# Kernel tuning notes

Hardware: AMD Instinct MI355X
Metric: run time of the kernel (lower is better)

The kernel has to match this reference:

```python
import jax, jax.numpy as jnp
import numpy as np

B, N, K = 16, 1024, 20
EPS = 1e-5

def _lin_init(key, fan_in, fan_out):
    k1, k2 = jax.random.split(key)
    s = 1.0 / np.sqrt(fan_in)
    W = jax.random.uniform(k1, (fan_in, fan_out), minval=-s, maxval=s, dtype=jnp.float32)
    b = jax.random.uniform(k2, (fan_out,), minval=-s, maxval=s, dtype=jnp.float32)
    return W, b

def setup_inputs() -> dict:
    key = jax.random.key(0)
    ks = jax.random.split(key, 12)
    pos = jax.random.normal(ks[0], (B * N, 3), dtype=jnp.float32)
    batch = jnp.repeat(jnp.arange(B, dtype=jnp.int64), N)
    W1a, b1a = _lin_init(ks[1], 6, 64);    W1b, b1b = _lin_init(ks[2], 64, 64)
    W2a, b2a = _lin_init(ks[3], 128, 64);  W2b, b2b = _lin_init(ks[4], 64, 64)
    W3a, b3a = _lin_init(ks[5], 128, 128); W3b, b3b = _lin_init(ks[6], 128, 128)
    W4a, b4a = _lin_init(ks[7], 256, 256); W4b, b4b = _lin_init(ks[8], 256, 256)
    lin1_w, lin1_b = _lin_init(ks[9], 512, 1024)
    gamma = jnp.ones((1024,), jnp.float32); beta = jnp.zeros((1024,), jnp.float32)
    lin2_w, lin2_b = _lin_init(ks[10], 1024, 40)
    return dict(pos=pos, batch=batch,
                W1a=W1a, b1a=b1a, W1b=W1b, b1b=b1b,
                W2a=W2a, b2a=b2a, W2b=W2b, b2b=b2b,
                W3a=W3a, b3a=b3a, W3b=W3b, b3b=b3b,
                W4a=W4a, b4a=b4a, W4b=W4b, b4b=b4b,
                lin1_w=lin1_w, lin1_b=lin1_b, gamma=gamma, beta=beta,
                lin2_w=lin2_w, lin2_b=lin2_b)

def _edge_conv(x, Wa, ba, Wb, bb):
    # x: [B, N, C]. Dynamic kNN in feature space (per cloud, self included,
    # matching PyG knn), edge feature [x_i, x_j - x_i], MLP, max-aggregate.
    sq = jnp.sum(x * x, axis=-1)                                   # [B,N]
    d = sq[:, :, None] - 2.0 * jnp.einsum('bnc,bmc->bnm', x, x) + sq[:, None, :]
    _, idx = jax.lax.top_k(-d, K)                                  # [B,N,K]
    xj = jax.vmap(lambda xb, ib: xb[ib])(x, idx)                   # [B,N,K,C]
    xi = jnp.broadcast_to(x[:, :, None, :], xj.shape)
    e = jnp.concatenate([xi, xj - xi], axis=-1)                    # [B,N,K,2C]
    h = jax.nn.relu(e @ Wa + ba) @ Wb + bb                         # [B,N,K,Co]
    return jnp.max(h, axis=2)                                      # [B,N,Co]

def reference(pos, batch, W1a, b1a, W1b, b1b, W2a, b2a, W2b, b2b,
              W3a, b3a, W3b, b3b, W4a, b4a, W4b, b4b,
              lin1_w, lin1_b, gamma, beta, lin2_w, lin2_b):
    del batch  # clouds are equal-sized: batch == repeat(arange(B), N)
    x = pos.reshape(B, N, 3)
    x1 = _edge_conv(x,  W1a, b1a, W1b, b1b)   # [B,N,64]
    x2 = _edge_conv(x1, W2a, b2a, W2b, b2b)   # [B,N,64]
    x3 = _edge_conv(x2, W3a, b3a, W3b, b3b)   # [B,N,128]
    x4 = _edge_conv(x3, W4a, b4a, W4b, b4b)   # [B,N,256]
    x_cat = jnp.concatenate([x1, x2, x3, x4], axis=-1)  # [B,N,512]
    pooled = jnp.max(x_cat, axis=1)                      # global_max_pool -> [B,512]
    h = pooled @ lin1_w + lin1_b                         # [B,1024]
    mu = jnp.mean(h, axis=0)
    var = jnp.mean((h - mu) ** 2, axis=0)                # biased, as PyTorch BN
    h = (h - mu) * jax.lax.rsqrt(var + EPS) * gamma + beta
    h = jax.nn.relu(h)                                   # dropout is identity in eval
    logits = h @ lin2_w + lin2_b                         # [B,40]
    return jax.nn.log_softmax(logits, axis=1)
```

## Files before the change

kernel.cpp:

```cpp
#include <hip/hip_runtime.h>
#include <hip/hip_bf16.h>
#include <hip/hip_fp16.h>

#define B_   16
#define N_   1024
#define KNN  20
#define NP   (B_ * N_)

typedef short bf16x8 __attribute__((ext_vector_type(8)));
typedef _Float16 half8 __attribute__((ext_vector_type(8)));
typedef float f32x4  __attribute__((ext_vector_type(4)));
typedef float f32x16 __attribute__((ext_vector_type(16)));

__device__ __forceinline__ unsigned short f2bf(float f) {
  unsigned u = __float_as_uint(f);
  u += 0x7fffu + ((u >> 16) & 1u);
  return (unsigned short)(u >> 16);
}

__global__ __launch_bounds__(256) void pairdist_kernel(
    const float* __restrict__ X, int LD, int coff, int C,
    unsigned* __restrict__ Dk) {
  __shared__ __align__(16) char pd_smem[64 * 68 * 4];
  __shared__ float sqi_s[64], sqj_s[64];
  float (*Xi)[68] = (float(*)[68])pd_smem;
  float (*Xj)[68] = (float(*)[68])(pd_smem + 32 * 68 * 4);
  unsigned (*Tt)[68] = (unsigned(*)[68])pd_smem;
  int lin = blockIdx.x, by = 0;
  while (lin >= 16 - by) { lin -= 16 - by; ++by; }
  int bx = by + lin;
  int b  = blockIdx.z;
  int i0 = by * 64, j0 = bx * 64;
  int t  = threadIdx.x;
  int tx = t & 15, ty = t >> 4;
  int cx = t & 31, ry = t >> 5;
  float acc[4][4] = {};
  float sqacc = 0.f;
  for (int c0 = 0; c0 < C; c0 += 32) {
    int cc = min(32, C - c0);
    if (cx < cc) {
      for (int r = ry; r < 64; r += 8) {
        Xi[cx][r] = X[(size_t)(b * N_ + i0 + r) * LD + coff + c0 + cx];
        Xj[cx][r] = X[(size_t)(b * N_ + j0 + r) * LD + coff + c0 + cx];
      }
    }
    __syncthreads();
    if (t < 64) {
      for (int c = 0; c < cc; ++c) sqacc = fmaf(Xi[c][t], Xi[c][t], sqacc);
    } else if (t < 128) {
      int r = t - 64;
      for (int c = 0; c < cc; ++c) sqacc = fmaf(Xj[c][r], Xj[c][r], sqacc);
    }
    for (int c = 0; c < cc; ++c) {
      float4 a4 = *(const float4*)&Xi[c][ty * 4];
      float4 b4 = *(const float4*)&Xj[c][tx * 4];
      float a[4] = {a4.x, a4.y, a4.z, a4.w};
      float bb[4] = {b4.x, b4.y, b4.z, b4.w};
#pragma unroll
      for (int p = 0; p < 4; ++p)
#pragma unroll
        for (int q = 0; q < 4; ++q)
          acc[p][q] = fmaf(a[p], bb[q], acc[p][q]);
    }
    __syncthreads();
  }
  if (t < 64) sqi_s[t] = sqacc;
  else if (t < 128) sqj_s[t - 64] = sqacc;
  __syncthreads();
  float sqi[4], sqj[4];
#pragma unroll
  for (int p = 0; p < 4; ++p) sqi[p] = sqi_s[ty * 4 + p];
#pragma unroll
  for (int q = 0; q < 4; ++q) sqj[q] = sqj_s[tx * 4 + q];
  bool offdiag = (bx > by);
#pragma unroll
  for (int p = 0; p < 4; ++p) {
    uint4 st;
    unsigned* kk = (unsigned*)&st;
#pragma unroll
    for (int q = 0; q < 4; ++q) {
      float d = fmaxf((sqi[p] - 2.f * acc[p][q]) + sqj[q], 0.f);
      unsigned db = __float_as_uint(d) & 0xFFFFFC00u;
      kk[q] = db | (unsigned)(j0 + tx * 4 + q);
      if (offdiag)
        Tt[tx * 4 + q][ty * 4 + p] = db | (unsigned)(i0 + ty * 4 + p);
    }
    *(uint4*)&Dk[(size_t)(b * N_ + i0 + ty * 4 + p) * N_ + j0 + tx * 4] = st;
  }
  if (offdiag) {
    __syncthreads();
#pragma unroll
    for (int p = 0; p < 4; ++p) {
      *(uint4*)&Dk[(size_t)(b * N_ + j0 + ty * 4 + p) * N_ + i0 + tx * 4] =
          *(uint4*)&Tt[ty * 4 + p][tx * 4];
    }
  }
}

template<int C>
__global__ __launch_bounds__(256) void sqc_kernel(
    const float* __restrict__ X, int coff, float* __restrict__ sq) {
  int w = threadIdx.x >> 6, lane = threadIdx.x & 63;
  int pt = blockIdx.x * 4 + w;
  const float* xr = X + (size_t)pt * 512 + coff;
  float s = 0.f;
  for (int c = lane; c < C; c += 64) s = fmaf(xr[c], xr[c], s);
#pragma unroll
  for (int off = 32; off >= 1; off >>= 1) s += __shfl_xor(s, off);
  if (lane == 0) sq[pt] = s;
}

template<int C>
__global__ __launch_bounds__(256) void gramt_kernel(
    const float* __restrict__ X, int coff, const float* __restrict__ sqv,
    unsigned* __restrict__ Dk) {
  constexpr int KP = C / 64;
  __shared__ __align__(16) unsigned short Phi[64 * 64], Plo[64 * 64];
  __shared__ __align__(16) unsigned short Qhi[64 * 64], Qlo[64 * 64];
  int tid = threadIdx.x, wv = tid >> 6, lane = tid & 63;
  int rc = lane & 31, half = lane >> 5;
  int ti = blockIdx.x & 15, tj = blockIdx.x >> 4;
  int b  = blockIdx.z;
  int qi = wv >> 1, qj = wv & 1;
  f32x16 acc = {};
#pragma unroll
  for (int kp = 0; kp < KP; ++kp) {
    if (kp) __syncthreads();
#pragma unroll
    for (int it = 0; it < 4; ++it) {
      int u = tid + it * 256;
      int side = u >> 9;
      int row  = (u >> 3) & 63;
      int slot = u & 7;
      int grow = b * N_ + (side ? tj : ti) * 64 + row;
      const float* xr = X + (size_t)grow * 512 + coff + kp * 64 + slot * 8;
      float4 x0 = *(const float4*)xr;
      float4 x1 = *(const float4*)(xr + 4);
      float xs[8] = {x0.x, x0.y, x0.z, x0.w, x1.x, x1.y, x1.z, x1.w};
      union { half8 v; _Float16 h[8]; } H, L;
#pragma unroll
      for (int q = 0; q < 8; ++q) {
        _Float16 hv = (_Float16)xs[q];
        H.h[q] = hv;
        L.h[q] = (_Float16)(xs[q] - (float)hv);
      }
      int off = row * 64 + (slot ^ (row & 7)) * 8;
      if (side) { *(half8*)&Qhi[off] = H.v; *(half8*)&Qlo[off] = L.v; }
      else      { *(half8*)&Phi[off] = H.v; *(half8*)&Plo[off] = L.v; }
    }
    __syncthreads();
#pragma unroll
    for (int ch = 0; ch < 4; ++ch) {
      int s = ch * 2 + half;
      int arow = qi * 32 + rc, brow = qj * 32 + rc;
      int aoff = arow * 64 + (s ^ (arow & 7)) * 8;
      int boff = brow * 64 + (s ^ (brow & 7)) * 8;
      half8 Ah = *(const half8*)&Phi[aoff];
      half8 Al = *(const half8*)&Plo[aoff];
      half8 Bh = *(const half8*)&Qhi[boff];
      half8 Bl = *(const half8*)&Qlo[boff];
      acc = __builtin_amdgcn_mfma_f32_32x32x16_f16(Ah, Bh, acc, 0, 0, 0);
      acc = __builtin_amdgcn_mfma_f32_32x32x16_f16(Al, Bh, acc, 0, 0, 0);
      acc = __builtin_amdgcn_mfma_f32_32x32x16_f16(Ah, Bl, acc, 0, 0, 0);
    }
  }
  int gj = tj * 64 + qj * 32 + rc;
  float sqj = sqv[b * N_ + gj];
#pragma unroll
  for (int e = 0; e < 16; ++e) {
    int gi = ti * 64 + qi * 32 + (e & 3) + 8 * (e >> 2) + 4 * half;
    float sqi = sqv[b * N_ + gi];
    float d = fmaxf(sqi - 2.f * acc[e] + sqj, 0.f);
    if (gi == gj) d = 0.f;
    Dk[(size_t)(b * N_ + gi) * N_ + gj] =
        (__float_as_uint(d) & 0xFFFFFC00u) | (unsigned)gj;
  }
}

__device__ __forceinline__ unsigned wave_min_bcast(unsigned x) {
  unsigned t;
  t = (unsigned)__builtin_amdgcn_update_dpp(-1, (int)x, 0x111, 0xF, 0xF, false);
  x = min(x, t);
  t = (unsigned)__builtin_amdgcn_update_dpp(-1, (int)x, 0x112, 0xF, 0xF, false);
  x = min(x, t);
  t = (unsigned)__builtin_amdgcn_update_dpp(-1, (int)x, 0x114, 0xF, 0xF, false);
  x = min(x, t);
  t = (unsigned)__builtin_amdgcn_update_dpp(-1, (int)x, 0x118, 0xF, 0xF, false);
  x = min(x, t);
  t = (unsigned)__builtin_amdgcn_update_dpp(-1, (int)x, 0x142, 0xF, 0xF, false);
  x = min(x, t);
  t = (unsigned)__builtin_amdgcn_update_dpp(-1, (int)x, 0x143, 0xF, 0xF, false);
  x = min(x, t);
  return (unsigned)__builtin_amdgcn_readlane((int)x, 63);
}

__global__ __launch_bounds__(256) void topk_kernel(
    const unsigned* __restrict__ Dk, int* __restrict__ idx) {
  int w = threadIdx.x >> 6, lane = threadIdx.x & 63;
  int p = blockIdx.x * 4 + w;
  const unsigned* row = Dk + (size_t)p * N_;
  unsigned key[16];
#pragma unroll
  for (int s = 0; s < 16; ++s) key[s] = row[lane + 64 * s];
  int base = p & ~(N_ - 1);
  for (int k = 0; k < KNN; ++k) {
    unsigned m = key[0];
#pragma unroll
    for (int s = 1; s < 16; ++s) m = min(m, key[s]);
    unsigned gm = wave_min_bcast(m);
    int j = (int)(gm & 1023u);
    if (lane == 0) idx[p * KNN + k] = base + j;
    if ((j & 63) == lane) key[j >> 6] = 0xFFFFFFFFu;
  }
}

__global__ __launch_bounds__(256) void transform_kernel(
    const float* __restrict__ X, int LD, int coff, int Cin, int Cmid,
    const float* __restrict__ Wa, const float* __restrict__ ba,
    unsigned short* __restrict__ u, unsigned short* __restrict__ v) {
  __shared__ float xs[16 * 128];
  int w = threadIdx.x >> 6, lane = threadIdx.x & 63;
  int m  = blockIdx.y * 64 + lane;
  int p0 = blockIdx.x * 16;
  for (int i = threadIdx.x; i < 16 * Cin; i += 256) {
    int pt = i / Cin, c = i - pt * Cin;
    xs[pt * Cin + c] = X[(size_t)(p0 + pt) * LD + coff + c];
  }
  __syncthreads();
  const float* xw = xs + (w * 4) * Cin;
  float ua[4] = {0.f, 0.f, 0.f, 0.f}, va[4] = {0.f, 0.f, 0.f, 0.f};
  for (int c = 0; c < Cin; ++c) {
    float wt = Wa[(size_t)c * Cmid + m];
    float wb = Wa[(size_t)(Cin + c) * Cmid + m];
    float wd = wt - wb;
#pragma unroll
    for (int i = 0; i < 4; ++i) {
      float xv = xw[i * Cin + c];
      ua[i] = fmaf(xv, wd, ua[i]);
      va[i] = fmaf(xv, wb, va[i]);
    }
  }
  float bias = ba[m];
#pragma unroll
  for (int i = 0; i < 4; ++i) {
    u[(size_t)(p0 + w * 4 + i) * Cmid + m] = f2bf(ua[i] + bias);
    v[(size_t)(p0 + w * 4 + i) * Cmid + m] = f2bf(va[i]);
  }
}

__global__ __launch_bounds__(256) void cvtwa_swz_kernel(
    const float* __restrict__ A2, const float* __restrict__ A3,
    const float* __restrict__ A4,
    unsigned short* __restrict__ d2, unsigned short* __restrict__ b2,
    unsigned short* __restrict__ d3, unsigned short* __restrict__ b3,
    unsigned short* __restrict__ d4, unsigned short* __restrict__ b4) {
  int z = blockIdx.z;
  const float* Wa; unsigned short *wd, *wb; int Cin, Cmid;
  if (z == 0)      { Wa = A2; wd = d2; wb = b2; Cin = 64;  Cmid = 64;  }
  else if (z == 1) { Wa = A3; wd = d3; wb = b3; Cin = 64;  Cmid = 128; }
  else             { Wa = A4; wd = d4; wb = b4; Cin = 128; Cmid = 256; }
  int KC = Cin / 16;
  int NC = (Cmid / 32) * KC * 64;
  int ci = blockIdx.x * 256 + threadIdx.x;
  if (ci >= NC) return;
  int ntc = ci >> 6, lane = ci & 63;
  int nt = ntc / KC, c = ntc - nt * KC;
  int n  = nt * 32 + (lane & 31);
  int kb = c * 16 + (lane >> 5) * 8;
#pragma unroll
  for (int j = 0; j < 8; ++j) {
    float top = Wa[(size_t)(kb + j) * Cmid + n];
    float bot = Wa[(size_t)(Cin + kb + j) * Cmid + n];
    wd[(size_t)ci * 8 + j] = f2bf(top - bot);
    wb[(size_t)ci * 8 + j] = f2bf(bot);
  }
}

template<int Cin, int Cmid>
__global__ __launch_bounds__(256) void transform_mfma_kernel(
    const float* __restrict__ X, int LD, int coff,
    const unsigned short* __restrict__ wdf, const unsigned short* __restrict__ wbf,
    const float* __restrict__ ba,
    unsigned short* __restrict__ u, unsigned short* __restrict__ v) {
  constexpr int KC = Cin / 16;
  int wv = threadIdx.x >> 6, lane = threadIdx.x & 63;
  int row = lane & 31, half = lane >> 5;
  int p0 = blockIdx.x * 128 + wv * 32;
  int nt = blockIdx.y;

  bf16x8 afr[KC];
  const float* xr = X + (size_t)(p0 + row) * LD + coff + half * 8;
#pragma unroll
  for (int c = 0; c < KC; ++c) {
    float4 x0 = *(const float4*)(xr + c * 16);
    float4 x1 = *(const float4*)(xr + c * 16 + 4);
    union { bf16x8 vec; __hip_bfloat162 h[4]; } pk;
    pk.h[0] = __float22bfloat162_rn({x0.x, x0.y});
    pk.h[1] = __float22bfloat162_rn({x0.z, x0.w});
    pk.h[2] = __float22bfloat162_rn({x1.x, x1.y});
    pk.h[3] = __float22bfloat162_rn({x1.z, x1.w});
    afr[c] = pk.vec;
  }

  const unsigned short* wdl = wdf + ((size_t)nt * KC * 64 + lane) * 8;
  const unsigned short* wbl = wbf + ((size_t)nt * KC * 64 + lane) * 8;
  f32x16 au = {}, av = {};
#pragma unroll
  for (int c = 0; c < KC; ++c) {
    bf16x8 bd = *(const bf16x8*)(wdl + (size_t)c * 512);
    au = __builtin_amdgcn_mfma_f32_32x32x16_bf16(afr[c], bd, au, 0, 0, 0);
  }
#pragma unroll
  for (int c = 0; c < KC; ++c) {
    bf16x8 bv = *(const bf16x8*)(wbl + (size_t)c * 512);
    av = __builtin_amdgcn_mfma_f32_32x32x16_bf16(afr[c], bv, av, 0, 0, 0);
  }

  int m = nt * 32 + row;
  float bias = ba[m];
#pragma unroll
  for (int e = 0; e < 16; ++e) {
    int orow = (e & 3) + 8 * (e >> 2) + 4 * half;
    u[(size_t)(p0 + orow) * Cmid + m] = f2bf(au[e] + bias);
    v[(size_t)(p0 + orow) * Cmid + m] = f2bf(av[e]);
  }
}

__global__ __launch_bounds__(256) void cvtw4_kernel(
    const float* __restrict__ W0, const float* __restrict__ W1,
    const float* __restrict__ W2, const float* __restrict__ W3,
    unsigned short* __restrict__ o0, unsigned short* __restrict__ o1,
    unsigned short* __restrict__ o2, unsigned short* __restrict__ o3) {
  __shared__ unsigned short tile[32][33];
  int z = blockIdx.z;
  const float* W; unsigned short* out; int Cmid, Cout;
  if (z == 0)      { W = W0; out = o0; Cmid = 64;  Cout = 64;  }
  else if (z == 1) { W = W1; out = o1; Cmid = 64;  Cout = 64;  }
  else if (z == 2) { W = W2; out = o2; Cmid = 128; Cout = 128; }
  else             { W = W3; out = o3; Cmid = 256; Cout = 256; }
  int c0 = blockIdx.x * 32, co0 = blockIdx.y * 32;
  if (c0 >= Cmid || co0 >= Cout) return;
  int tx = threadIdx.x & 31, ty = threadIdx.x >> 5;
  for (int r = ty; r < 32; r += 8)
    tile[r][tx] = f2bf(W[(size_t)(c0 + r) * Cout + co0 + tx]);
  __syncthreads();
  for (int r = ty; r < 32; r += 8)
    out[(size_t)(co0 + r) * Cmid + c0 + tx] = tile[tx][r];
}

template<int Cmid, int Cout, int CG>
__global__ __launch_bounds__(960, 3) void edge_mlp_kernel(
    const unsigned short* __restrict__ u, const unsigned short* __restrict__ v,
    const int* __restrict__ idx,
    const unsigned short* __restrict__ wbt, const float* __restrict__ bb,
    float* __restrict__ xcat, int coff) {
  constexpr int AP = Cmid + 8;
  constexpr int T  = CG / 32;
  constexpr int KC = Cmid / 16;
  constexpr int G  = Cout / CG;
  __shared__ __align__(16) unsigned short W_lds[CG * AP];
  __shared__ float qmax[120 * CG];
  int tid = threadIdx.x, w = tid >> 6, lane = tid & 63;
  int col = lane & 31, half = lane >> 5;

  int rg = blockIdx.x * 480 + w * 32 + col;
  int rgc = min(rg, NP * KNN - 1);
  int p  = rgc / 20;
  int j  = idx[rgc];
  const unsigned short* up = u + (size_t)p * Cmid + half * 8;
  const unsigned short* vp = v + (size_t)j * Cmid + half * 8;

  bf16x8 afr[KC];
#pragma unroll
  for (int c = 0; c < KC; ++c) {
    union { int4 i; __hip_bfloat162 h[4]; bf16x8 vec; } U, V, R;
    U.i = *(const int4*)(up + c * 16);
    V.i = *(const int4*)(vp + c * 16);
#pragma unroll
    for (int q = 0; q < 4; ++q) {
      float2 a = __bfloat1622float2(U.h[q]);
      float2 b = __bfloat1622float2(V.h[q]);
      R.h[q] = __float22bfloat162_rn({fmaxf(a.x + b.x, 0.f), fmaxf(a.y + b.y, 0.f)});
    }
    afr[c] = R.vec;
  }

  int brow = col * AP + half * 8;

  for (int g = 0; g < G; ++g) {
    __syncthreads();
    for (int i = tid; i < CG * (Cmid / 8); i += 960) {
      int rr = i / (Cmid / 8), q = i - rr * (Cmid / 8);
      *(int4*)&W_lds[rr * AP + q * 8] =
          *(const int4*)&wbt[(size_t)(g * CG + rr) * Cmid + q * 8];
    }
    __syncthreads();
    f32x16 acc[T] = {};
#pragma unroll
    for (int c = 0; c < KC; ++c) {
#pragma unroll
      for (int t = 0; t < T; ++t) {
        bf16x8 bf = *(const bf16x8*)&W_lds[brow + t * 32 * AP + c * 16];
        acc[t] = __builtin_amdgcn_mfma_f32_32x32x16_bf16(afr[c], bf, acc[t], 0, 0, 0);
      }
    }
#pragma unroll
    for (int t = 0; t < T; ++t) {
#pragma unroll
      for (int Q = 0; Q < 4; ++Q) {
        float m0 = fmaxf(fmaxf(acc[t][4 * Q], acc[t][4 * Q + 1]),
                         fmaxf(acc[t][4 * Q + 2], acc[t][4 * Q + 3]));
        qmax[(w * 8 + 2 * Q + half) * CG + t * 32 + col] = m0;
      }
    }
    __syncthreads();
    for (int i = tid; i < 24 * CG; i += 960) {
      int pl = i / CG, c2 = i - pl * CG;
      int pg = blockIdx.x * 24 + pl;
      if (pg < NP) {
        float mm = qmax[(pl * 5 + 0) * CG + c2];
#pragma unroll
        for (int qq = 1; qq < 5; ++qq) mm = fmaxf(mm, qmax[(pl * 5 + qq) * CG + c2]);
        xcat[(size_t)pg * 512 + coff + g * CG + c2] = mm + bb[g * CG + c2];
      }
    }
  }
}

__global__ __launch_bounds__(256) void pool1_kernel(const float* __restrict__ xcat,
                                                    float* __restrict__ part) {
  int b = blockIdx.x, g = blockIdx.y, t = threadIdx.x;
  const float* base = xcat + ((size_t)b * N_ + g * 128) * 512 + t * 2;
  float mx = -__builtin_inff(), my = -__builtin_inff();
#pragma unroll 4
  for (int r = 0; r < 128; ++r) {
    float2 vv = *(const float2*)(base + (size_t)r * 512);
    mx = fmaxf(mx, vv.x);
    my = fmaxf(my, vv.y);
  }
  *(float2*)&part[((size_t)b * 8 + g) * 512 + t * 2] = make_float2(mx, my);
}

__global__ __launch_bounds__(256) void pool2_kernel(const float* __restrict__ part,
                                                    float* __restrict__ pooled) {
  int b = blockIdx.x, t = threadIdx.x;
  float2 m = *(const float2*)&part[(size_t)b * 8 * 512 + t * 2];
#pragma unroll
  for (int g = 1; g < 8; ++g) {
    float2 vv = *(const float2*)&part[((size_t)b * 8 + g) * 512 + t * 2];
    m.x = fmaxf(m.x, vv.x);
    m.y = fmaxf(m.y, vv.y);
  }
  *(float2*)&pooled[b * 512 + t * 2] = m;
}

__global__ __launch_bounds__(256) void lin1_kernel(const float* __restrict__ pooled,
                                                   const float* __restrict__ W,
                                                   const float* __restrict__ bias,
                                                   float* __restrict__ h) {
  int flat = blockIdx.x * 256 + threadIdx.x;
  int b = flat >> 10, m = flat & 1023;
  float s = 0.f;
  for (int c = 0; c < 512; ++c) s = fmaf(pooled[b * 512 + c], W[(size_t)c * 1024 + m], s);
  h[flat] = s + bias[m];
}

__global__ __launch_bounds__(256) void bn_kernel(const float* __restrict__ h,
                                                 const float* __restrict__ gamma,
                                                 const float* __restrict__ beta,
                                                 float* __restrict__ h2) {
  int m = blockIdx.x * 256 + threadIdx.x;
  float s = 0.f;
  for (int b = 0; b < 16; ++b) s += h[b * 1024 + m];
  float mu = s * (1.f / 16.f);
  float vv = 0.f;
  for (int b = 0; b < 16; ++b) { float d = h[b * 1024 + m] - mu; vv = fmaf(d, d, vv); }
  vv *= (1.f / 16.f);
  float rstd = rsqrtf(vv + 1e-5f);
  float g = gamma[m] * rstd, be = beta[m];
  for (int b = 0; b < 16; ++b) {
    float val = (h[b * 1024 + m] - mu) * g + be;
    h2[b * 1024 + m] = fmaxf(val, 0.f);
  }
}

__global__ __launch_bounds__(64) void lin2_kernel(const float* __restrict__ h2,
                                                  const float* __restrict__ W,
                                                  const float* __restrict__ bias,
                                                  float* __restrict__ out) {
  int b = blockIdx.x, lane = threadIdx.x;
  float logit = 0.f;
  if (lane < 40) {
    logit = bias[lane];
    for (int c = 0; c < 1024; ++c)
      logit = fmaf(h2[b * 1024 + c], W[(size_t)c * 40 + lane], logit);
  }
  float mv = (lane < 40) ? logit : -__builtin_inff();
#pragma unroll
  for (int off = 32; off >= 1; off >>= 1) mv = fmaxf(mv, __shfl_xor(mv, off));
  float e = (lane < 40) ? expf(logit - mv) : 0.f;
#pragma unroll
  for (int off = 32; off >= 1; off >>= 1) e += __shfl_xor(e, off);
  float lse = mv + logf(e);
  if (lane < 40) out[b * 40 + lane] = logit - lse;
}

extern "C" void kernel_launch(void* const* d_in, const int* in_sizes, int n_in,
                              void* d_out, int out_size, void* d_ws, size_t ws_size,
                              hipStream_t stream) {
  const float* pos    = (const float*)d_in[0];
  const float* W1a = (const float*)d_in[2];  const float* b1a = (const float*)d_in[3];
  const float* W1b = (const float*)d_in[4];  const float* b1b = (const float*)d_in[5];
  const float* W2a = (const float*)d_in[6];  const float* b2a = (const float*)d_in[7];
  const float* W2b = (const float*)d_in[8];  const float* b2b = (const float*)d_in[9];
  const float* W3a = (const float*)d_in[10]; const float* b3a = (const float*)d_in[11];
  const float* W3b = (const float*)d_in[12]; const float* b3b = (const float*)d_in[13];
  const float* W4a = (const float*)d_in[14]; const float* b4a = (const float*)d_in[15];
  const float* W4b = (const float*)d_in[16]; const float* b4b = (const float*)d_in[17];
  const float* lin1_w = (const float*)d_in[18]; const float* lin1_b = (const float*)d_in[19];
  const float* gamma  = (const float*)d_in[20]; const float* beta   = (const float*)d_in[21];
  const float* lin2_w = (const float*)d_in[22]; const float* lin2_b = (const float*)d_in[23];
  float* out = (float*)d_out;

  char* ws = (char*)d_ws;
  size_t off = 0;
  auto alloc = [&](size_t bytes) {
    void* p = ws + off; off += (bytes + 255) & ~(size_t)255; return p;
  };
  float*    xcat = (float*)alloc((size_t)NP * 512 * 4);
  unsigned* Dk   = (unsigned*)alloc((size_t)NP * N_ * 4);
  int*      idx  = (int*)alloc((size_t)NP * KNN * 4);
  unsigned short* wbt1 = (unsigned short*)alloc(64 * 64 * 2);
  unsigned short* wbt2 = (unsigned short*)alloc(64 * 64 * 2);
  unsigned short* wbt3 = (unsigned short*)alloc(128 * 128 * 2);
  unsigned short* wbt4 = (unsigned short*)alloc(256 * 256 * 2);
  unsigned short* wd2 = (unsigned short*)alloc(64 * 64 * 2);
  unsigned short* wb2 = (unsigned short*)alloc(64 * 64 * 2);
  unsigned short* wd3 = (unsigned short*)alloc(64 * 128 * 2);
  unsigned short* wb3 = (unsigned short*)alloc(64 * 128 * 2);
  unsigned short* wd4 = (unsigned short*)alloc(128 * 256 * 2);
  unsigned short* wb4 = (unsigned short*)alloc(128 * 256 * 2);
  float* h      = (float*)alloc(16 * 1024 * 4);
  float* h2     = (float*)alloc(16 * 1024 * 4);
  float* pooled = (float*)alloc(16 * 512 * 4);
  float* part   = (float*)alloc(16 * 8 * 512 * 4);
  float* sqv    = (float*)alloc((size_t)NP * 4);
  unsigned short* u = (unsigned short*)Dk;
  unsigned short* v = (unsigned short*)Dk + (size_t)NP * 256;

  cvtw4_kernel<<<dim3(8, 8, 4), 256, 0, stream>>>(W1b, W2b, W3b, W4b,
                                                  wbt1, wbt2, wbt3, wbt4);
  cvtwa_swz_kernel<<<dim3(16, 1, 3), 256, 0, stream>>>(W2a, W3a, W4a,
                                                       wd2, wb2, wd3, wb3, wd4, wb4);

  dim3 pd_grid(136, 1, 16);
  dim3 gr_grid(256, 1, 16);
  const int EB = (NP * KNN + 479) / 480;
  pairdist_kernel<<<pd_grid, 256, 0, stream>>>(pos, 3, 0, 3, Dk);
  topk_kernel<<<NP / 4, 256, 0, stream>>>(Dk, idx);
  transform_kernel<<<dim3(NP / 16, 1), 256, 0, stream>>>(pos, 3, 0, 3, 64, W1a, b1a, u, v);
  edge_mlp_kernel<64, 64, 64><<<EB, 960, 0, stream>>>(u, v, idx, wbt1, b1b, xcat, 0);
  sqc_kernel<64><<<NP / 4, 256, 0, stream>>>(xcat, 0, sqv);
  gramt_kernel<64><<<gr_grid, 256, 0, stream>>>(xcat, 0, sqv, Dk);
  topk_kernel<<<NP / 4, 256, 0, stream>>>(Dk, idx);
  transform_mfma_kernel<64, 64><<<dim3(NP / 128, 2), 256, 0, stream>>>(
      xcat, 512, 0, wd2, wb2, b2a, u, v);
  edge_mlp_kernel<64, 64, 64><<<EB, 960, 0, stream>>>(u, v, idx, wbt2, b2b, xcat, 64);
  sqc_kernel<64><<<NP / 4, 256, 0, stream>>>(xcat, 64, sqv);
  gramt_kernel<64><<<gr_grid, 256, 0, stream>>>(xcat, 64, sqv, Dk);
  topk_kernel<<<NP / 4, 256, 0, stream>>>(Dk, idx);
  transform_mfma_kernel<64, 128><<<dim3(NP / 128, 4), 256, 0, stream>>>(
      xcat, 512, 64, wd3, wb3, b3a, u, v);
  edge_mlp_kernel<128, 128, 64><<<EB, 960, 0, stream>>>(u, v, idx, wbt3, b3b, xcat, 128);
  sqc_kernel<128><<<NP / 4, 256, 0, stream>>>(xcat, 128, sqv);
  gramt_kernel<128><<<gr_grid, 256, 0, stream>>>(xcat, 128, sqv, Dk);
  topk_kernel<<<NP / 4, 256, 0, stream>>>(Dk, idx);
  transform_mfma_kernel<128, 256><<<dim3(NP / 128, 8), 256, 0, stream>>>(
      xcat, 512, 128, wd4, wb4, b4a, u, v);
  edge_mlp_kernel<256, 256, 64><<<EB, 960, 0, stream>>>(u, v, idx, wbt4, b4b, xcat, 256);
  pool1_kernel<<<dim3(16, 8), 256, 0, stream>>>(xcat, part);
  pool2_kernel<<<16, 256, 0, stream>>>(part, pooled);
  lin1_kernel<<<64, 256, 0, stream>>>(pooled, lin1_w, lin1_b, h);
  bn_kernel<<<4, 256, 0, stream>>>(h, gamma, beta, h2);
  lin2_kernel<<<16, 64, 0, stream>>>(h2, lin2_w, lin2_b, out);
}
```

Measured before the change: 541.3 us.

## Exploit Gram matrix symmetry: compute upper-triangle tiles and write transposed copies

```diff
diff --git a/kernel.cpp b/kernel.cpp
--- a/kernel.cpp
+++ b/kernel.cpp
@@ -115,11 +115,17 @@
     const float* __restrict__ X, int coff, const float* __restrict__ sqv,
     unsigned* __restrict__ Dk) {
   constexpr int KP = C / 64;
-  __shared__ __align__(16) unsigned short Phi[64 * 64], Plo[64 * 64];
-  __shared__ __align__(16) unsigned short Qhi[64 * 64], Qlo[64 * 64];
+  __shared__ __align__(16) char gt_smem[32768];
+  unsigned short* Phi = (unsigned short*)gt_smem;
+  unsigned short* Plo = Phi + 4096;
+  unsigned short* Qhi = Plo + 4096;
+  unsigned short* Qlo = Qhi + 4096;
+  unsigned (*Tt)[68] = (unsigned(*)[68])gt_smem;
   int tid = threadIdx.x, wv = tid >> 6, lane = tid & 63;
   int rc = lane & 31, half = lane >> 5;
-  int ti = blockIdx.x & 15, tj = blockIdx.x >> 4;
+  int lin = blockIdx.x, ti = 0;
+  while (lin >= 16 - ti) { lin -= 16 - ti; ++ti; }
+  int tj = ti + lin;
   int b  = blockIdx.z;
   int qi = wv >> 1, qj = wv & 1;
   f32x16 acc = {};
@@ -164,16 +170,32 @@
       acc = __builtin_amdgcn_mfma_f32_32x32x16_f16(Ah, Bl, acc, 0, 0, 0);
     }
   }
+  __syncthreads();
+  bool offdiag = (tj > ti);
   int gj = tj * 64 + qj * 32 + rc;
   float sqj = sqv[b * N_ + gj];
 #pragma unroll
   for (int e = 0; e < 16; ++e) {
-    int gi = ti * 64 + qi * 32 + (e & 3) + 8 * (e >> 2) + 4 * half;
+    int erow = (e & 3) + 8 * (e >> 2) + 4 * half;
+    int gi = ti * 64 + qi * 32 + erow;
     float sqi = sqv[b * N_ + gi];
     float d = fmaxf(sqi - 2.f * acc[e] + sqj, 0.f);
     if (gi == gj) d = 0.f;
-    Dk[(size_t)(b * N_ + gi) * N_ + gj] =
-        (__float_as_uint(d) & 0xFFFFFC00u) | (unsigned)gj;
+    unsigned db = __float_as_uint(d) & 0xFFFFFC00u;
+    Dk[(size_t)(b * N_ + gi) * N_ + gj] = db | (unsigned)gj;
+    if (offdiag)
+      Tt[qj * 32 + rc][qi * 32 + erow] = db | (unsigned)gi;
+  }
+  if (offdiag) {
+    __syncthreads();
+#pragma unroll
+    for (int it = 0; it < 4; ++it) {
+      int u = tid + it * 256;
+      int r  = u >> 4;
+      int c4 = (u & 15) * 4;
+      uint4 vv = *(const uint4*)&Tt[r][c4];
+      *(uint4*)&Dk[(size_t)(b * N_ + tj * 64 + r) * N_ + ti * 64 + c4] = vv;
+    }
   }
 }
 
@@ -554,26 +576,26 @@
                                                        wd2, wb2, wd3, wb3, wd4, wb4);
 
   dim3 pd_grid(136, 1, 16);
-  dim3 gr_grid(256, 1, 16);
+  dim3 gt_grid(136, 1, 16);
   const int EB = (NP * KNN + 479) / 480;
   pairdist_kernel<<<pd_grid, 256, 0, stream>>>(pos, 3, 0, 3, Dk);
   topk_kernel<<<NP / 4, 256, 0, stream>>>(Dk, idx);
   transform_kernel<<<dim3(NP / 16, 1), 256, 0, stream>>>(pos, 3, 0, 3, 64, W1a, b1a, u, v);
   edge_mlp_kernel<64, 64, 64><<<EB, 960, 0, stream>>>(u, v, idx, wbt1, b1b, xcat, 0);
   sqc_kernel<64><<<NP / 4, 256, 0, stream>>>(xcat, 0, sqv);
-  gramt_kernel<64><<<gr_grid, 256, 0, stream>>>(xcat, 0, sqv, Dk);
+  gramt_kernel<64><<<gt_grid, 256, 0, stream>>>(xcat, 0, sqv, Dk);
   topk_kernel<<<NP / 4, 256, 0, stream>>>(Dk, idx);
   transform_mfma_kernel<64, 64><<<dim3(NP / 128, 2), 256, 0, stream>>>(
       xcat, 512, 0, wd2, wb2, b2a, u, v);
   edge_mlp_kernel<64, 64, 64><<<EB, 960, 0, stream>>>(u, v, idx, wbt2, b2b, xcat, 64);
   sqc_kernel<64><<<NP / 4, 256, 0, stream>>>(xcat, 64, sqv);
-  gramt_kernel<64><<<gr_grid, 256, 0, stream>>>(xcat, 64, sqv, Dk);
+  gramt_kernel<64><<<gt_grid, 256, 0, stream>>>(xcat, 64, sqv, Dk);
   topk_kernel<<<NP / 4, 256, 0, stream>>>(Dk, idx);
   transform_mfma_kernel<64, 128><<<dim3(NP / 128, 4), 256, 0, stream>>>(
       xcat, 512, 64, wd3, wb3, b3a, u, v);
   edge_mlp_kernel<128, 128, 64><<<EB, 960, 0, stream>>>(u, v, idx, wbt3, b3b, xcat, 128);
   sqc_kernel<128><<<NP / 4, 256, 0, stream>>>(xcat, 128, sqv);
-  gramt_kernel<128><<<gr_grid, 256, 0, stream>>>(xcat, 128, sqv, Dk);
+  gramt_kernel<128><<<gt_grid, 256, 0, stream>>>(xcat, 128, sqv, Dk);
   topk_kernel<<<NP / 4, 256, 0, stream>>>(Dk, idx);
   transform_mfma_kernel<128, 256><<<dim3(NP / 128, 8), 256, 0, stream>>>(
       xcat, 512, 128, wd4, wb4, b4a, u, v);
```

Result: no change. 541.3 us (-0.0%).
